# Optimization experiments

Measured on AMD Instinct MI355X. Metric: run time of the kernel, lower is better.

The kernel has to match this reference:

```python
import jax, jax.numpy as jnp
import numpy as np

U = 3  # GRU units

def _gru_scan(x, kernel, rec_kernel, bias):
    # x: [B, S, F]; kernel: [F, 3U]; rec_kernel: [U, 3U]; bias: [2, 3U]
    # Keras GRUCell with reset_after=True (TF2 default).
    B = x.shape[0]
    # Precompute all input projections in one big matmul: [B, S, 3U]
    xk = jnp.einsum('bsf,fg->bsg', x, kernel) + bias[0]
    xk = jnp.transpose(xk, (1, 0, 2))  # [S, B, 3U] for scan over time
    rec_bias = bias[1]

    def step(h, xt):
        inner = h @ rec_kernel + rec_bias                  # [B, 3U]
        xz, xr, xh = jnp.split(xt, 3, axis=-1)
        rz, rr, rh = jnp.split(inner, 3, axis=-1)
        z = jax.nn.sigmoid(xz + rz)
        r = jax.nn.sigmoid(xr + rr)
        hh = jnp.tanh(xh + r * rh)
        h_new = z * h + (1.0 - z) * hh
        return h_new, None

    h0 = jnp.zeros((B, U), dtype=x.dtype)
    h_final, _ = jax.lax.scan(step, h0, xk)
    return h_final  # [B, U]


def setup_inputs() -> dict:
    key = jax.random.key(0)
    ks = jax.random.split(key, 6)
    B, S, F = 4096, 256, 64
    return {
        'inputs': jax.random.normal(ks[0], (B, S, F), dtype=jnp.float32),
        'kernel': jax.random.normal(ks[1], (F, 3 * U), dtype=jnp.float32) * 0.1,
        'rec_kernel': jax.random.normal(ks[2], (U, 3 * U), dtype=jnp.float32) * 0.1,
        'bias': jax.random.normal(ks[3], (2, 3 * U), dtype=jnp.float32) * 0.1,
        'dense_w': jax.random.normal(ks[4], (U, 10), dtype=jnp.float32) * 0.1,
        'dense_b': jnp.zeros((10,), dtype=jnp.float32),
    }


def reference(inputs, kernel, rec_kernel, bias, dense_w, dense_b):
    h = _gru_scan(inputs, kernel, rec_kernel, bias)   # [B, U]; Flatten is a no-op
    logits = h @ dense_w + dense_b                     # [B, 10]
    return jax.nn.softmax(logits, axis=-1)
```

## Files before the change

### kernel.cpp

```cpp
#include <hip/hip_runtime.h>

#define BB 4096
#define SS 256
#define FF 64
#define GG 9

#define NEG_LOG2E -1.4426950408889634f
#define TWO_LOG2E  2.8853900817779268f

typedef float f2 __attribute__((ext_vector_type(2)));

#if __has_builtin(__builtin_amdgcn_exp2f)
__device__ __forceinline__ float fast_exp2(float x) { return __builtin_amdgcn_exp2f(x); }
#else
__device__ __forceinline__ float fast_exp2(float x) { return exp2f(x); }
#endif
#if __has_builtin(__builtin_amdgcn_rcpf)
__device__ __forceinline__ float fast_rcp(float x) { return __builtin_amdgcn_rcpf(x); }
#else
__device__ __forceinline__ float fast_rcp(float x) { return 1.0f / x; }
#endif

template <int CTRL>
__device__ __forceinline__ float dpp_f(float v) {
  return __int_as_float(
      __builtin_amdgcn_mov_dpp(__float_as_int(v), CTRL, 0xF, 0xF, true));
}

__global__ __launch_bounds__(64, 1) void fused_gru_kernel(
    const float* __restrict__ x,
    const float* __restrict__ kernel_w,
    const float* __restrict__ rec_kernel,
    const float* __restrict__ bias,
    const float* __restrict__ dense_w,
    const float* __restrict__ dense_b,
    float* __restrict__ out)
{
  const int lane = threadIdx.x;
  const int fl   = lane & 15;
  const int u    = lane & 3;
  const int uc   = (u < 3) ? u : 2;
  const int c    = blockIdx.x * 4 + (lane >> 4);

  f2 w01[4], w23[4], w45[4], w67[4];
  float w8[4];
#pragma unroll
  for (int e = 0; e < 4; ++e) {
    const float* kw = kernel_w + (fl * 4 + e) * GG;
    w01[e] = (f2){kw[0] * NEG_LOG2E, kw[1] * NEG_LOG2E};
    w23[e] = (f2){kw[2] * NEG_LOG2E, kw[3] * NEG_LOG2E};
    w45[e] = (f2){kw[4] * NEG_LOG2E, kw[5] * NEG_LOG2E};
    w67[e] = (f2){kw[6] * TWO_LOG2E, kw[7] * TWO_LOG2E};
    w8[e]  = kw[8] * TWO_LOG2E;
  }

  const float Q = 0.0625f;
  const f2 b01q = {(bias[0] + bias[GG + 0]) * NEG_LOG2E * Q,
                   (bias[1] + bias[GG + 1]) * NEG_LOG2E * Q};
  const f2 b23q = {(bias[2] + bias[GG + 2]) * NEG_LOG2E * Q,
                   (bias[3] + bias[GG + 3]) * NEG_LOG2E * Q};
  const f2 b45q = {(bias[4] + bias[GG + 4]) * NEG_LOG2E * Q,
                   (bias[5] + bias[GG + 5]) * NEG_LOG2E * Q};
  const f2 b67q = {bias[6] * TWO_LOG2E * Q, bias[7] * TWO_LOG2E * Q};
  const float b8q = bias[8] * TWO_LOG2E * Q;

  float wz[3], wr[3], wh[3];
#pragma unroll
  for (int hh = 0; hh < 3; ++hh) {
    wz[hh] = rec_kernel[hh * GG + uc]     * NEG_LOG2E;
    wr[hh] = rec_kernel[hh * GG + 3 + uc] * NEG_LOG2E;
    wh[hh] = rec_kernel[hh * GG + 6 + uc] * TWO_LOG2E;
  }
  const float rbh = bias[GG + 6 + uc] * TWO_LOG2E;

  float h0 = 0.0f, h1 = 0.0f, h2 = 0.0f, hprev = 0.0f;

  const float4* pc = reinterpret_cast<const float4*>(x) + (size_t)c * SS * 16 + fl;

  float4 X0, X1, X2, X3, X4, X5, X6, X7;

  auto step = [&](const float4 v) {
    f2 a01 = b01q, a23 = b23q, a45 = b45q, a67 = b67q;
    float a8 = b8q;
    a01 = v.x * w01[0] + a01; a23 = v.x * w23[0] + a23;
    a45 = v.x * w45[0] + a45; a67 = v.x * w67[0] + a67;
    a8 = fmaf(v.x, w8[0], a8);
    a01 = v.y * w01[1] + a01; a23 = v.y * w23[1] + a23;
    a45 = v.y * w45[1] + a45; a67 = v.y * w67[1] + a67;
    a8 = fmaf(v.y, w8[1], a8);
    a01 = v.z * w01[2] + a01; a23 = v.z * w23[2] + a23;
    a45 = v.z * w45[2] + a45; a67 = v.z * w67[2] + a67;
    a8 = fmaf(v.z, w8[2], a8);
    a01 = v.w * w01[3] + a01; a23 = v.w * w23[3] + a23;
    a45 = v.w * w45[3] + a45; a67 = v.w * w67[3] + a67;
    a8 = fmaf(v.w, w8[3], a8);

    float s0 = a01.x, s1 = a01.y, s2 = a23.x, s3 = a23.y, s4 = a45.x,
          s5 = a45.y, s6 = a67.x, s7 = a67.y, s8 = a8;
    s0 += dpp_f<0xB1>(s0); s1 += dpp_f<0xB1>(s1); s2 += dpp_f<0xB1>(s2);
    s3 += dpp_f<0xB1>(s3); s4 += dpp_f<0xB1>(s4); s5 += dpp_f<0xB1>(s5);
    s6 += dpp_f<0xB1>(s6); s7 += dpp_f<0xB1>(s7); s8 += dpp_f<0xB1>(s8);
    s0 += dpp_f<0x4E>(s0); s1 += dpp_f<0x4E>(s1); s2 += dpp_f<0x4E>(s2);
    s3 += dpp_f<0x4E>(s3); s4 += dpp_f<0x4E>(s4); s5 += dpp_f<0x4E>(s5);
    s6 += dpp_f<0x4E>(s6); s7 += dpp_f<0x4E>(s7); s8 += dpp_f<0x4E>(s8);

    float az = (u == 0) ? s0 : ((u == 1) ? s1 : s2);
    float ar = (u == 0) ? s3 : ((u == 1) ? s4 : s5);
    float sh = (u == 0) ? s6 : ((u == 1) ? s7 : s8);

    az += dpp_f<0x124>(az); ar += dpp_f<0x124>(ar); sh += dpp_f<0x124>(sh);
    az += dpp_f<0x128>(az); ar += dpp_f<0x128>(ar); sh += dpp_f<0x128>(sh);

    const float iz = fmaf(h2, wz[2], fmaf(h1, wz[1], fmaf(h0, wz[0], az)));
    const float ir = fmaf(h2, wr[2], fmaf(h1, wr[1], fmaf(h0, wr[0], ar)));
    const float ih = fmaf(h2, wh[2], fmaf(h1, wh[1], fmaf(h0, wh[0], rbh)));
    const float z = fast_rcp(1.0f + fast_exp2(iz));
    const float r = fast_rcp(1.0f + fast_exp2(ir));
    const float t = fmaf(-2.0f, fast_rcp(1.0f + fast_exp2(fmaf(r, ih, sh))), 1.0f);
    const float hn = fmaf(z, hprev - t, t);
    hprev = hn;
    h0 = dpp_f<0x00>(hn);
    h1 = dpp_f<0x55>(hn);
    h2 = dpp_f<0xAA>(hn);
  };

  auto pf = [&](int sn) -> float4 {
    sn = (sn < SS) ? sn : (SS - 1);
    return pc[(size_t)sn * 16];
  };

  X0 = pf(0); X1 = pf(1); X2 = pf(2); X3 = pf(3);
  X4 = pf(4); X5 = pf(5); X6 = pf(6); X7 = pf(7);

  for (int sg = 0; sg < SS; sg += 8) {
    step(X0); X0 = pf(sg + 8);
    step(X1); X1 = pf(sg + 9);
    step(X2); X2 = pf(sg + 10);
    step(X3); X3 = pf(sg + 11);
    step(X4); X4 = pf(sg + 12);
    step(X5); X5 = pf(sg + 13);
    step(X6); X6 = pf(sg + 14);
    step(X7); X7 = pf(sg + 15);
  }

  if (fl < 4) {
    float lg[10];
#pragma unroll
    for (int j = 0; j < 10; ++j)
      lg[j] = dense_b[j] + h0 * dense_w[j] + h1 * dense_w[10 + j] + h2 * dense_w[20 + j];
    float m = lg[0];
#pragma unroll
    for (int j = 1; j < 10; ++j) m = fmaxf(m, lg[j]);
    float e[10];
    float ssum = 0.0f;
#pragma unroll
    for (int j = 0; j < 10; ++j) {
      e[j] = fast_exp2(1.4426950408889634f * (lg[j] - m));
      ssum += e[j];
    }
    const float inv = fast_rcp(ssum);
#pragma unroll
    for (int j = u; j < 10; j += 4) out[(size_t)c * 10 + j] = e[j] * inv;
  }
}

extern "C" void kernel_launch(void* const* d_in, const int* in_sizes, int n_in,
                              void* d_out, int out_size, void* d_ws, size_t ws_size,
                              hipStream_t stream) {
  const float* x      = (const float*)d_in[0];
  const float* kern   = (const float*)d_in[1];
  const float* rkern  = (const float*)d_in[2];
  const float* bias   = (const float*)d_in[3];
  const float* dw     = (const float*)d_in[4];
  const float* db     = (const float*)d_in[5];
  float* out = (float*)d_out;

  fused_gru_kernel<<<BB / 4, 64, 0, stream>>>(x, kern, rkern, bias, dw, db, out);
}
```

Measured before the change: 54.68 us.

## Repartition input projection so each lane owns one gate unit over 16 features

Changes the work split within each 16-lane group. Before, each lane took 4 features and computed all 9 gate sums, which needed a 4-lane butterfly reduction plus a select. Now each lane covers one gate unit over 16 features, so each step needs only the 2-stage row reduction over 4 lanes. This removes most of the DPP shuffles and per-step reduction work. The cost is four float4 loads per step per lane, a prefetch depth cut from 8 steps to 4, more weight registers, and redundant compute on the fourth lane of each quad.

```diff
diff --git a/kernel.cpp b/kernel.cpp
--- a/kernel.cpp
+++ b/kernel.cpp
@@ -37,32 +37,25 @@
     float* __restrict__ out)
 {
   const int lane = threadIdx.x;
-  const int fl   = lane & 15;
-  const int u    = lane & 3;
+  const int l16  = lane & 15;
+  const int u    = l16 & 3;
   const int uc   = (u < 3) ? u : 2;
+  const int q    = l16 >> 2;
   const int c    = blockIdx.x * 4 + (lane >> 4);
 
-  f2 w01[4], w23[4], w45[4], w67[4];
-  float w8[4];
+  f2 wzr[16];
+  float wh_[16];
 #pragma unroll
-  for (int e = 0; e < 4; ++e) {
-    const float* kw = kernel_w + (fl * 4 + e) * GG;
-    w01[e] = (f2){kw[0] * NEG_LOG2E, kw[1] * NEG_LOG2E};
-    w23[e] = (f2){kw[2] * NEG_LOG2E, kw[3] * NEG_LOG2E};
-    w45[e] = (f2){kw[4] * NEG_LOG2E, kw[5] * NEG_LOG2E};
-    w67[e] = (f2){kw[6] * TWO_LOG2E, kw[7] * TWO_LOG2E};
-    w8[e]  = kw[8] * TWO_LOG2E;
+  for (int e = 0; e < 16; ++e) {
+    const float* kw = kernel_w + (16 * q + e) * GG;
+    wzr[e] = (f2){kw[uc] * NEG_LOG2E, kw[3 + uc] * NEG_LOG2E};
+    wh_[e] = kw[6 + uc] * TWO_LOG2E;
   }
 
-  const float Q = 0.0625f;
-  const f2 b01q = {(bias[0] + bias[GG + 0]) * NEG_LOG2E * Q,
-                   (bias[1] + bias[GG + 1]) * NEG_LOG2E * Q};
-  const f2 b23q = {(bias[2] + bias[GG + 2]) * NEG_LOG2E * Q,
-                   (bias[3] + bias[GG + 3]) * NEG_LOG2E * Q};
-  const f2 b45q = {(bias[4] + bias[GG + 4]) * NEG_LOG2E * Q,
-                   (bias[5] + bias[GG + 5]) * NEG_LOG2E * Q};
-  const f2 b67q = {bias[6] * TWO_LOG2E * Q, bias[7] * TWO_LOG2E * Q};
-  const float b8q = bias[8] * TWO_LOG2E * Q;
+  const float Q = 0.25f;
+  const f2 bzr = {(bias[uc] + bias[GG + uc]) * NEG_LOG2E * Q,
+                  (bias[3 + uc] + bias[GG + 3 + uc]) * NEG_LOG2E * Q};
+  const float bh = bias[6 + uc] * TWO_LOG2E * Q;
 
   float wz[3], wr[3], wh[3];
 #pragma unroll
@@ -75,39 +68,31 @@
 
   float h0 = 0.0f, h1 = 0.0f, h2 = 0.0f, hprev = 0.0f;
 
-  const float4* pc = reinterpret_cast<const float4*>(x) + (size_t)c * SS * 16 + fl;
+  const float* pX = x + (size_t)c * SS * FF + 16 * q;
 
-  float4 X0, X1, X2, X3, X4, X5, X6, X7;
+  float4 X0[4], X1[4], X2[4], X3[4];
+  auto ldt = [&](float4 (&R)[4], int s) {
+    const float* p = pX + (size_t)s * FF;
+    R[0] = *reinterpret_cast<const float4*>(p);
+    R[1] = *reinterpret_cast<const float4*>(p + 4);
+    R[2] = *reinterpret_cast<const float4*>(p + 8);
+    R[3] = *reinterpret_cast<const float4*>(p + 12);
+  };
 
-  auto step = [&](const float4 v) {
-    f2 a01 = b01q, a23 = b23q, a45 = b45q, a67 = b67q;
-    float a8 = b8q;
-    a01 = v.x * w01[0] + a01; a23 = v.x * w23[0] + a23;
-    a45 = v.x * w45[0] + a45; a67 = v.x * w67[0] + a67;
-    a8 = fmaf(v.x, w8[0], a8);
-    a01 = v.y * w01[1] + a01; a23 = v.y * w23[1] + a23;
-    a45 = v.y * w45[1] + a45; a67 = v.y * w67[1] + a67;
-    a8 = fmaf(v.y, w8[1], a8);
-    a01 = v.z * w01[2] + a01; a23 = v.z * w23[2] + a23;
-    a45 = v.z * w45[2] + a45; a67 = v.z * w67[2] + a67;
-    a8 = fmaf(v.z, w8[2], a8);
-    a01 = v.w * w01[3] + a01; a23 = v.w * w23[3] + a23;
-    a45 = v.w * w45[3] + a45; a67 = v.w * w67[3] + a67;
-    a8 = fmaf(v.w, w8[3], a8);
+  auto step = [&](const float4 (&V)[4]) {
+    f2 azr = bzr;
+    float sh = bh;
+#pragma unroll
+    for (int j = 0; j < 4; ++j) {
+      const float4 v = V[j];
+      const int e = j * 4;
+      azr = v.x * wzr[e + 0] + azr; sh = fmaf(v.x, wh_[e + 0], sh);
+      azr = v.y * wzr[e + 1] + azr; sh = fmaf(v.y, wh_[e + 1], sh);
+      azr = v.z * wzr[e + 2] + azr; sh = fmaf(v.z, wh_[e + 2], sh);
+      azr = v.w * wzr[e + 3] + azr; sh = fmaf(v.w, wh_[e + 3], sh);
+    }
 
-    float s0 = a01.x, s1 = a01.y, s2 = a23.x, s3 = a23.y, s4 = a45.x,
-          s5 = a45.y, s6 = a67.x, s7 = a67.y, s8 = a8;
-    s0 += dpp_f<0xB1>(s0); s1 += dpp_f<0xB1>(s1); s2 += dpp_f<0xB1>(s2);
-    s3 += dpp_f<0xB1>(s3); s4 += dpp_f<0xB1>(s4); s5 += dpp_f<0xB1>(s5);
-    s6 += dpp_f<0xB1>(s6); s7 += dpp_f<0xB1>(s7); s8 += dpp_f<0xB1>(s8);
-    s0 += dpp_f<0x4E>(s0); s1 += dpp_f<0x4E>(s1); s2 += dpp_f<0x4E>(s2);
-    s3 += dpp_f<0x4E>(s3); s4 += dpp_f<0x4E>(s4); s5 += dpp_f<0x4E>(s5);
-    s6 += dpp_f<0x4E>(s6); s7 += dpp_f<0x4E>(s7); s8 += dpp_f<0x4E>(s8);
-
-    float az = (u == 0) ? s0 : ((u == 1) ? s1 : s2);
-    float ar = (u == 0) ? s3 : ((u == 1) ? s4 : s5);
-    float sh = (u == 0) ? s6 : ((u == 1) ? s7 : s8);
-
+    float az = azr.x, ar = azr.y;
     az += dpp_f<0x124>(az); ar += dpp_f<0x124>(ar); sh += dpp_f<0x124>(sh);
     az += dpp_f<0x128>(az); ar += dpp_f<0x128>(ar); sh += dpp_f<0x128>(sh);
 
@@ -124,26 +109,17 @@
     h2 = dpp_f<0xAA>(hn);
   };
 
-  auto pf = [&](int sn) -> float4 {
-    sn = (sn < SS) ? sn : (SS - 1);
-    return pc[(size_t)sn * 16];
-  };
+  auto clampi = [](int sn) { return (sn < SS) ? sn : (SS - 1); };
 
-  X0 = pf(0); X1 = pf(1); X2 = pf(2); X3 = pf(3);
-  X4 = pf(4); X5 = pf(5); X6 = pf(6); X7 = pf(7);
-
-  for (int sg = 0; sg < SS; sg += 8) {
-    step(X0); X0 = pf(sg + 8);
-    step(X1); X1 = pf(sg + 9);
-    step(X2); X2 = pf(sg + 10);
-    step(X3); X3 = pf(sg + 11);
-    step(X4); X4 = pf(sg + 12);
-    step(X5); X5 = pf(sg + 13);
-    step(X6); X6 = pf(sg + 14);
-    step(X7); X7 = pf(sg + 15);
+  ldt(X0, 0); ldt(X1, 1); ldt(X2, 2); ldt(X3, 3);
+  for (int sg = 0; sg < SS; sg += 4) {
+    step(X0); ldt(X0, clampi(sg + 4));
+    step(X1); ldt(X1, clampi(sg + 5));
+    step(X2); ldt(X2, clampi(sg + 6));
+    step(X3); ldt(X3, clampi(sg + 7));
   }
 
-  if (fl < 4) {
+  if (l16 < 4) {
     float lg[10];
 #pragma unroll
     for (int j = 0; j < 10; ++j)
```

Result: slower. 77.55 us (+41.8%).

## Split GRU into producer and consumer wavefronts with double-buffered LDS tiles

Applied to the files above, without the earlier changes.

The single wavefront per block becomes two. One wave computes the input projections for a 16-step tile and writes them to double-buffered shared memory, while the other wave runs the serial recurrent gate chain on the previous tile. The aim is to take the projection FMAs and DPP reductions off the latency-critical recurrence path. The cost is a block barrier per tile, LDS traffic, and twice the threads per block.

```diff
diff --git a/kernel.cpp b/kernel.cpp
--- a/kernel.cpp
+++ b/kernel.cpp
@@ -4,6 +4,8 @@
 #define SS 256
 #define FF 64
 #define GG 9
+#define TT 16
+#define NT (SS / TT)
 
 #define NEG_LOG2E -1.4426950408889634f
 #define TWO_LOG2E  2.8853900817779268f
@@ -27,7 +29,7 @@
       __builtin_amdgcn_mov_dpp(__float_as_int(v), CTRL, 0xF, 0xF, true));
 }
 
-__global__ __launch_bounds__(64, 1) void fused_gru_kernel(
+__global__ __launch_bounds__(128, 2) void fused_gru_kernel(
     const float* __restrict__ x,
     const float* __restrict__ kernel_w,
     const float* __restrict__ rec_kernel,
@@ -36,24 +38,28 @@
     const float* __restrict__ dense_b,
     float* __restrict__ out)
 {
-  const int lane = threadIdx.x;
-  const int fl   = lane & 15;
-  const int u    = lane & 3;
-  const int uc   = (u < 3) ? u : 2;
-  const int c    = blockIdx.x * 4 + (lane >> 4);
+  __shared__ float lds[2][TT][4][12];
+
+  const int tid = threadIdx.x;
+  const int wid = tid >> 6;
+  const int l   = tid & 63;
+  const int l16 = l & 15;
+  const int u   = l16 & 3;
+  const int uc  = (u < 3) ? u : 2;
+  const int row = l >> 4;
+  const int c   = blockIdx.x * 4 + row;
 
   f2 w01[4], w23[4], w45[4], w67[4];
   float w8[4];
 #pragma unroll
   for (int e = 0; e < 4; ++e) {
-    const float* kw = kernel_w + (fl * 4 + e) * GG;
+    const float* kw = kernel_w + (l16 * 4 + e) * GG;
     w01[e] = (f2){kw[0] * NEG_LOG2E, kw[1] * NEG_LOG2E};
     w23[e] = (f2){kw[2] * NEG_LOG2E, kw[3] * NEG_LOG2E};
     w45[e] = (f2){kw[4] * NEG_LOG2E, kw[5] * NEG_LOG2E};
     w67[e] = (f2){kw[6] * TWO_LOG2E, kw[7] * TWO_LOG2E};
     w8[e]  = kw[8] * TWO_LOG2E;
   }
-
   const float Q = 0.0625f;
   const f2 b01q = {(bias[0] + bias[GG + 0]) * NEG_LOG2E * Q,
                    (bias[1] + bias[GG + 1]) * NEG_LOG2E * Q};
@@ -64,22 +70,14 @@
   const f2 b67q = {bias[6] * TWO_LOG2E * Q, bias[7] * TWO_LOG2E * Q};
   const float b8q = bias[8] * TWO_LOG2E * Q;
 
-  float wz[3], wr[3], wh[3];
-#pragma unroll
-  for (int hh = 0; hh < 3; ++hh) {
-    wz[hh] = rec_kernel[hh * GG + uc]     * NEG_LOG2E;
-    wr[hh] = rec_kernel[hh * GG + 3 + uc] * NEG_LOG2E;
-    wh[hh] = rec_kernel[hh * GG + 6 + uc] * TWO_LOG2E;
-  }
-  const float rbh = bias[GG + 6 + uc] * TWO_LOG2E;
-
-  float h0 = 0.0f, h1 = 0.0f, h2 = 0.0f, hprev = 0.0f;
-
-  const float4* pc = reinterpret_cast<const float4*>(x) + (size_t)c * SS * 16 + fl;
-
+  const float4* pc = reinterpret_cast<const float4*>(x) + (size_t)c * SS * 16 + l16;
   float4 X0, X1, X2, X3, X4, X5, X6, X7;
-
-  auto step = [&](const float4 v) {
+  auto pf = [&](int sn) -> float4 {
+    sn = (sn < SS) ? sn : (SS - 1);
+    return pc[(size_t)sn * 16];
+  };
+
+  auto produce_step = [&](const float4 v, int s) {
     f2 a01 = b01q, a23 = b23q, a45 = b45q, a67 = b67q;
     float a8 = b8q;
     a01 = v.x * w01[0] + a01; a23 = v.x * w23[0] + a23;
@@ -107,10 +105,37 @@
     float az = (u == 0) ? s0 : ((u == 1) ? s1 : s2);
     float ar = (u == 0) ? s3 : ((u == 1) ? s4 : s5);
     float sh = (u == 0) ? s6 : ((u == 1) ? s7 : s8);
-
     az += dpp_f<0x124>(az); ar += dpp_f<0x124>(ar); sh += dpp_f<0x124>(sh);
     az += dpp_f<0x128>(az); ar += dpp_f<0x128>(ar); sh += dpp_f<0x128>(sh);
 
+    if (l16 < 3) {
+      float* p = &lds[(s >> 4) & 1][s & 15][row][l16 * 3];
+      p[0] = az; p[1] = ar; p[2] = sh;
+    }
+  };
+
+  auto prod8 = [&](int sb) {
+    produce_step(X0, sb + 0); X0 = pf(sb + 8);
+    produce_step(X1, sb + 1); X1 = pf(sb + 9);
+    produce_step(X2, sb + 2); X2 = pf(sb + 10);
+    produce_step(X3, sb + 3); X3 = pf(sb + 11);
+    produce_step(X4, sb + 4); X4 = pf(sb + 12);
+    produce_step(X5, sb + 5); X5 = pf(sb + 13);
+    produce_step(X6, sb + 6); X6 = pf(sb + 14);
+    produce_step(X7, sb + 7); X7 = pf(sb + 15);
+  };
+
+  float wz[3], wr[3], wh[3];
+#pragma unroll
+  for (int hh = 0; hh < 3; ++hh) {
+    wz[hh] = rec_kernel[hh * GG + uc]     * NEG_LOG2E;
+    wr[hh] = rec_kernel[hh * GG + 3 + uc] * NEG_LOG2E;
+    wh[hh] = rec_kernel[hh * GG + 6 + uc] * TWO_LOG2E;
+  }
+  const float rbh = bias[GG + 6 + uc] * TWO_LOG2E;
+  float h0 = 0.0f, h1 = 0.0f, h2 = 0.0f, hprev = 0.0f;
+
+  auto gate = [&](float az, float ar, float sh) {
     const float iz = fmaf(h2, wz[2], fmaf(h1, wz[1], fmaf(h0, wz[0], az)));
     const float ir = fmaf(h2, wr[2], fmaf(h1, wr[1], fmaf(h0, wr[0], ar)));
     const float ih = fmaf(h2, wh[2], fmaf(h1, wh[1], fmaf(h0, wh[0], rbh)));
@@ -124,26 +149,35 @@
     h2 = dpp_f<0xAA>(hn);
   };
 
-  auto pf = [&](int sn) -> float4 {
-    sn = (sn < SS) ? sn : (SS - 1);
-    return pc[(size_t)sn * 16];
-  };
-
-  X0 = pf(0); X1 = pf(1); X2 = pf(2); X3 = pf(3);
-  X4 = pf(4); X5 = pf(5); X6 = pf(6); X7 = pf(7);
-
-  for (int sg = 0; sg < SS; sg += 8) {
-    step(X0); X0 = pf(sg + 8);
-    step(X1); X1 = pf(sg + 9);
-    step(X2); X2 = pf(sg + 10);
-    step(X3); X3 = pf(sg + 11);
-    step(X4); X4 = pf(sg + 12);
-    step(X5); X5 = pf(sg + 13);
-    step(X6); X6 = pf(sg + 14);
-    step(X7); X7 = pf(sg + 15);
-  }
-
-  if (fl < 4) {
+  auto consume_tile = [&](int t) {
+    const float* pb = &lds[t & 1][0][row][uc * 3];
+    float azv[TT], arv[TT], shv[TT];
+#pragma unroll
+    for (int k = 0; k < TT; ++k) {
+      azv[k] = pb[k * 48 + 0];
+      arv[k] = pb[k * 48 + 1];
+      shv[k] = pb[k * 48 + 2];
+    }
+#pragma unroll
+    for (int k = 0; k < TT; ++k) gate(azv[k], arv[k], shv[k]);
+  };
+
+  if (wid == 0) {
+    X0 = pf(0); X1 = pf(1); X2 = pf(2); X3 = pf(3);
+    X4 = pf(4); X5 = pf(5); X6 = pf(6); X7 = pf(7);
+    prod8(0); prod8(8);
+  }
+  __syncthreads();
+  for (int t = 0; t < NT; ++t) {
+    if (wid == 0) {
+      if (t + 1 < NT) { prod8(TT * (t + 1)); prod8(TT * (t + 1) + 8); }
+    } else {
+      consume_tile(t);
+    }
+    __syncthreads();
+  }
+
+  if (wid == 1 && l16 < 4) {
     float lg[10];
 #pragma unroll
     for (int j = 0; j < 10; ++j)
@@ -175,5 +209,5 @@
   const float* db     = (const float*)d_in[5];
   float* out = (float*)d_out;
 
-  fused_gru_kernel<<<BB / 4, 64, 0, stream>>>(x, kern, rkern, bias, dw, db, out);
+  fused_gru_kernel<<<BB / 4, 128, 0, stream>>>(x, kern, rkern, bias, dw, db, out);
 }
```

Measured after the change: 64.34 us. 17.7% more time.
